# Kernel optimization log

Hardware: AMD Instinct MI355X
Metric: run time of the kernel (lower is better)

The kernel has to match this reference:

```python
import jax, jax.numpy as jnp
import numpy as np

B, T, C, H = 8, 2048, 1024, 64

def setup_inputs() -> dict:
    key = jax.random.key(0)
    kx, kq, kk, kv = jax.random.split(key, 4)
    scale = 1.0 / np.sqrt(C)
    return {
        "x": jax.random.normal(kx, (B, T, C), dtype=jnp.float32),
        "Wq": jax.random.normal(kq, (C, H), dtype=jnp.float32) * scale,
        "Wk": jax.random.normal(kk, (C, H), dtype=jnp.float32) * scale,
        "Wv": jax.random.normal(kv, (C, H), dtype=jnp.float32) * scale,
    }

def reference(x, Wq, Wk, Wv):
    # q,k,v: [B,T,H]
    q = jnp.einsum('btc,ch->bth', x, Wq)
    k = jnp.einsum('btc,ch->bth', x, Wk)
    v = jnp.einsum('btc,ch->bth', x, Wv)
    scale = k.shape[-1] ** -0.5
    wei = jnp.einsum('bth,bsh->bts', q, k) * scale  # [B,T,T]
    causal = jnp.tril(jnp.ones((x.shape[1], x.shape[1]), dtype=bool))
    wei = jnp.where(causal, wei, -jnp.inf)
    wei = jax.nn.softmax(wei, axis=-1)
    out = jnp.einsum('bts,bsh->bth', wei, v)  # [B,T,H]
    return out
```

## Files before the change

### kernel.cpp

```cpp
#include <hip/hip_runtime.h>

#define B_ 8
#define T_ 2048
#define C_ 1024
#define H_ 64

typedef __bf16 bf16x8 __attribute__((ext_vector_type(8)));
typedef float  f32x4  __attribute__((ext_vector_type(4)));
typedef unsigned short u16x8 __attribute__((ext_vector_type(8)));

__device__ __forceinline__ unsigned short f2bf(float f) {
    unsigned u = __builtin_bit_cast(unsigned, f);
    u += 0x8000u;
    return (unsigned short)(u >> 16);
}

__device__ __forceinline__ float bf2f(unsigned short v) {
    unsigned u = ((unsigned)v) << 16;
    return __builtin_bit_cast(float, u);
}

__device__ __forceinline__ unsigned pack2(float lo, float hi) {
    unsigned a = __builtin_bit_cast(unsigned, lo) + 0x8000u;
    unsigned b = __builtin_bit_cast(unsigned, hi) + 0x8000u;
    return (a >> 16) | (b & 0xffff0000u);
}

union U8 { unsigned u32[4]; u16x8 v; };

__device__ __forceinline__ u16x8 cvt8(float4 f0, float4 f1) {
    U8 r;
    r.u32[0] = pack2(f0.x, f0.y);
    r.u32[1] = pack2(f0.z, f0.w);
    r.u32[2] = pack2(f1.x, f1.y);
    r.u32[3] = pack2(f1.z, f1.w);
    return r.v;
}

__device__ __forceinline__ bf16x8 load8_bf(const unsigned short* p) {
    return __builtin_bit_cast(bf16x8, *(const u16x8*)p);
}


__global__ void cast_weights(const float* __restrict__ Wq,
                             const float* __restrict__ Wk,
                             const float* __restrict__ Wv,
                             unsigned short* __restrict__ Wtf) {
    int idx = blockIdx.x * blockDim.x + threadIdx.x;
    int n   = idx % 192;
    int c   = idx / 192;
    int w   = n >> 6;
    int h   = n & 63;
    const float* W = (w == 0) ? Wq : (w == 1) ? Wk : Wv;
    int nt = n >> 4, l16 = n & 15;
    int kc = c >> 5, quad = (c >> 3) & 3, j = c & 7;
    Wtf[(size_t)(nt * 32 + kc) * 512 + l16 * 32 + quad * 8 + j] =
        f2bf(W[(size_t)c * H_ + h]);
}

__global__ __launch_bounds__(512) void qkv_proj(
        const float* __restrict__ x,
        const unsigned short* __restrict__ Wtf,
        unsigned short* __restrict__ Qf,
        unsigned short* __restrict__ Kf,
        unsigned short* __restrict__ Vf) {
    __shared__ __attribute__((aligned(16))) unsigned short As_[32 * 1024];

    const int tid  = threadIdx.x;
    const int wave = tid >> 6;
    const int lane = tid & 63;
    const int l16  = lane & 15;
    const int quad = lane >> 4;
    const int ms   = wave >> 2;
    const int ns   = wave & 3;
    const size_t r0 = (size_t)blockIdx.x * 32;

#pragma unroll
    for (int i = 0; i < 8; i++) {
        int c   = i * 512 + tid;
        int row = c >> 7;
        int g   = c & 127;
        const float* p = x + (r0 + row) * C_ + g * 8;
        float4 f0 = *(const float4*)p;
        float4 f1 = *(const float4*)(p + 4);
        int off = row * 1024 + ((g & ~7) + ((g & 7) ^ (row & 7))) * 8;
        *(u16x8*)(&As_[off]) = cvt8(f0, f1);
    }
    __syncthreads();

    f32x4 acc[3];
#pragma unroll
    for (int i = 0; i < 3; i++) acc[i] = (f32x4){0.f, 0.f, 0.f, 0.f};

    const int arow = ms * 16 + l16;
    const int sw   = l16 & 7;
    const int loff = l16 * 32 + quad * 8;
    const unsigned short* wb = Wtf + (size_t)(ns * 3) * 32 * 512;

#pragma unroll 4
    for (int kc = 0; kc < 32; kc++) {
        int g = kc * 4 + quad;
        bf16x8 a = load8_bf(&As_[arow * 1024 + ((g & ~7) + ((g & 7) ^ sw)) * 8]);
#pragma unroll
        for (int i = 0; i < 3; i++) {
            bf16x8 b = load8_bf(wb + (size_t)(i * 32 + kc) * 512 + loff);
            acc[i] = __builtin_amdgcn_mfma_f32_16x16x32_bf16(a, b, acc[i], 0, 0, 0);
        }
    }

#pragma unroll
    for (int i = 0; i < 3; i++) {
        int nt = ns * 3 + i;
#pragma unroll
        for (int r = 0; r < 4; r++) {
            int row  = (int)r0 + ms * 16 + quad * 4 + r;
            int bb   = row >> 11;
            int tloc = row & (T_ - 1);
            unsigned short bv = f2bf(acc[i][r]);
            if (nt < 4) {
                int part  = nt >> 1;
                int quadf = (nt & 1) * 2 + (l16 >> 3);
                Qf[((size_t)(bb * 128 + (tloc >> 4)) * 2 + part) * 512
                   + (tloc & 15) * 32 + quadf * 8 + (l16 & 7)] = bv;
            } else if (nt < 8) {
                int nk    = nt - 4;
                int part  = nk >> 1;
                int quadf = (nk & 1) * 2 + (l16 >> 3);
                Kf[((size_t)(bb * 128 + (tloc >> 4)) * 2 + part) * 512
                   + (tloc & 15) * 32 + quadf * 8 + (l16 & 7)] = bv;
            } else {
                int ht  = nt - 8;
                int s32 = tloc >> 5;
                int w32 = tloc & 31;
                Vf[((size_t)(bb * 64 + s32) * 4 + ht) * 512
                   + l16 * 32 + (w32 >> 3) * 8 + (w32 & 7)] = bv;
            }
        }
    }
}

#define PROW 33
#define OMS2 66

__global__ __launch_bounds__(512) void attn(
        const unsigned short* __restrict__ Qf,
        const unsigned short* __restrict__ Kf,
        const unsigned short* __restrict__ Vf,
        float* __restrict__ out) {
    __shared__ unsigned int ps_[8 * 16 * PROW];
    __shared__ unsigned short Om_[8 * 16 * OMS2];
    __shared__ float mred_[8 * 16];
    __shared__ float lred_[8 * 16];

    const int tid  = threadIdx.x;
    const int wave = tid >> 6;
    const int lane = tid & 63;
    const int l16  = lane & 15;
    const int quad = lane >> 4;
    const int b    = blockIdx.x & 7;
    const int qt   = blockIdx.x >> 3;
    const int q0   = qt * 16;
    const int tdiag = qt >> 2;

    const int loff = l16 * 32 + quad * 8;

    const unsigned short* Qfb = Qf + (size_t)(b * 128 + qt) * 1024;
    bf16x8 qf0 = load8_bf(Qfb + loff);
    bf16x8 qf1 = load8_bf(Qfb + 512 + loff);

    f32x4 o[4];
#pragma unroll
    for (int i = 0; i < 4; i++) o[i] = (f32x4){0.f, 0.f, 0.f, 0.f};
    float m_run = -1e30f, l_run = 0.f;

    const float scale = 0.125f;
    const unsigned short* Kfb = Kf + (size_t)b * 128 * 1024;
    const unsigned short* Vfb = Vf + (size_t)b * 64 * 2048;
    unsigned int* Pw = &ps_[wave * 16 * PROW];

    for (int t = wave; t <= tdiag; t += 8) {
        bf16x8 vf[8];
#pragma unroll
        for (int ks = 0; ks < 2; ks++)
#pragma unroll
            for (int ht = 0; ht < 4; ht++)
                vf[ht * 2 + ks] = load8_bf(
                    Vfb + ((size_t)(t * 2 + ks) * 4 + ht) * 512 + loff);

        f32x4 s[4];
#pragma unroll
        for (int nt = 0; nt < 4; nt++) {
            const unsigned short* kp = Kfb + (size_t)(t * 4 + nt) * 1024;
            bf16x8 kf0 = load8_bf(kp + loff);
            bf16x8 kf1 = load8_bf(kp + 512 + loff);
            f32x4 z = (f32x4){0.f, 0.f, 0.f, 0.f};
            z = __builtin_amdgcn_mfma_f32_16x16x32_bf16(kf0, qf0, z, 0, 0, 0);
            z = __builtin_amdgcn_mfma_f32_16x16x32_bf16(kf1, qf1, z, 0, 0, 0);
            s[nt] = z;
        }

#pragma unroll
        for (int nt = 0; nt < 4; nt++)
#pragma unroll
            for (int r = 0; r < 4; r++) s[nt][r] *= scale;

        if (t == tdiag) {
#pragma unroll
            for (int nt = 0; nt < 4; nt++) {
#pragma unroll
                for (int r = 0; r < 4; r++) {
                    int key = t * 64 + nt * 16 + quad * 4 + r;
                    if (key > q0 + l16) s[nt][r] = -1e30f;
                }
            }
        }

        float mx;
        {
            float m0 = fmaxf(fmaxf(s[0][0], s[0][1]), fmaxf(s[0][2], s[0][3]));
            float m1 = fmaxf(fmaxf(s[1][0], s[1][1]), fmaxf(s[1][2], s[1][3]));
            float m2 = fmaxf(fmaxf(s[2][0], s[2][1]), fmaxf(s[2][2], s[2][3]));
            float m3 = fmaxf(fmaxf(s[3][0], s[3][1]), fmaxf(s[3][2], s[3][3]));
            mx = fmaxf(fmaxf(m0, m1), fmaxf(m2, m3));
        }
        mx = fmaxf(mx, __shfl_xor(mx, 16));
        mx = fmaxf(mx, __shfl_xor(mx, 32));
        const float m_new = fmaxf(m_run, mx);
        const float alpha = __expf(m_run - m_new);
        m_run = m_new;

        float rs = 0.f;
#pragma unroll
        for (int nt = 0; nt < 4; nt++) {
#pragma unroll
            for (int i = 0; i < 2; i++) {
                float p0 = __expf(s[nt][2 * i]     - m_new);
                float p1 = __expf(s[nt][2 * i + 1] - m_new);
                rs += p0 + p1;
                Pw[l16 * PROW + nt * 8 + quad * 2 + i] = pack2(p0, p1);
            }
        }
        rs += __shfl_xor(rs, 16);
        rs += __shfl_xor(rs, 32);
        l_run = l_run * alpha + rs;

#pragma unroll
        for (int ht = 0; ht < 4; ht++)
#pragma unroll
            for (int r = 0; r < 4; r++) o[ht][r] *= alpha;

#pragma unroll
        for (int ks = 0; ks < 2; ks++) {
            bf16x8 pB = __builtin_bit_cast(bf16x8,
                *(const u16x8*)(&Pw[l16 * PROW + ks * 16 + quad * 4]));
#pragma unroll
            for (int ht = 0; ht < 4; ht++)
                o[ht] = __builtin_amdgcn_mfma_f32_16x16x32_bf16(
                    vf[ht * 2 + ks], pB, o[ht], 0, 0, 0);
        }
    }

#pragma unroll
    for (int ht = 0; ht < 4; ht++)
#pragma unroll
        for (int r = 0; r < 4; r++)
            Om_[(wave * 16 + l16) * OMS2 + ht * 16 + quad * 4 + r] = f2bf(o[ht][r]);
    if (quad == 0) {
        mred_[wave * 16 + l16] = m_run;
        lred_[wave * 16 + l16] = l_run;
    }
    __syncthreads();

    const int hcol = tid & 63;
    const int qrow0 = tid >> 6;
#pragma unroll
    for (int qq = 0; qq < 2; qq++) {
        const int q = qrow0 + qq * 8;
        float M = -1e30f;
#pragma unroll
        for (int w = 0; w < 8; w++) M = fmaxf(M, mred_[w * 16 + q]);
        float lt = 0.f, ov = 0.f;
#pragma unroll
        for (int w = 0; w < 8; w++) {
            float e = __expf(mred_[w * 16 + q] - M);
            lt += e * lred_[w * 16 + q];
            ov += e * bf2f(Om_[(w * 16 + q) * OMS2 + hcol]);
        }
        out[((size_t)b * T_ + q0 + q) * H_ + hcol] = ov / lt;
    }
}

extern "C" void kernel_launch(void* const* d_in, const int* in_sizes, int n_in,
                              void* d_out, int out_size, void* d_ws, size_t ws_size,
                              hipStream_t stream) {
    const float* x  = (const float*)d_in[0];
    const float* Wq = (const float*)d_in[1];
    const float* Wk = (const float*)d_in[2];
    const float* Wv = (const float*)d_in[3];
    float* out = (float*)d_out;

    unsigned short* Qf  = (unsigned short*)d_ws;
    unsigned short* Kf  = Qf + (size_t)B_ * T_ * H_;
    unsigned short* Vf  = Kf + (size_t)B_ * T_ * H_;
    unsigned short* Wtf = Vf + (size_t)B_ * T_ * H_;

    cast_weights<<<(192 * C_) / 256, 256, 0, stream>>>(Wq, Wk, Wv, Wtf);
    qkv_proj<<<B_ * T_ / 32, 512, 0, stream>>>(x, Wtf, Qf, Kf, Vf);
    attn<<<B_ * (T_ / 16), 512, 0, stream>>>(Qf, Kf, Vf, out);
}
```

Measured before the change: 141.9 us.

## Reuse weight and K/V fragments across two row tiles and stage projection output

The QKV projection now uses 4 waves, each computing both 16-row halves. Each weight fragment therefore feeds two MFMAs, and x is staged in two K-halves to halve LDS use. Results are staged through LDS and written out as coalesced 16-byte stores instead of scattered 2-byte stores. Attention blocks now cover 32 queries with 4 waves, so each K/V fragment load serves two query groups. The cost is more registers per thread and fewer waves splitting the key range, which lengthens the per-wave serial loop.

Measured after the change: 141.4 us. No clear change (-0.3%).

```diff
diff --git a/kernel.cpp b/kernel.cpp
--- a/kernel.cpp
+++ b/kernel.cpp
@@ -53,104 +53,128 @@
     int h   = n & 63;
     const float* W = (w == 0) ? Wq : (w == 1) ? Wk : Wv;
     int nt = n >> 4, l16 = n & 15;
-    int kc = c >> 5, quad = (c >> 3) & 3, j = c & 7;
-    Wtf[(size_t)(nt * 32 + kc) * 512 + l16 * 32 + quad * 8 + j] =
+    int kk = c >> 5, quad = (c >> 3) & 3, j = c & 7;
+    Wtf[(size_t)(nt * 32 + kk) * 512 + l16 * 32 + quad * 8 + j] =
         f2bf(W[(size_t)c * H_ + h]);
 }
 
-__global__ __launch_bounds__(512) void qkv_proj(
+__global__ __launch_bounds__(256) void qkv_proj(
         const float* __restrict__ x,
         const unsigned short* __restrict__ Wtf,
         unsigned short* __restrict__ Qf,
         unsigned short* __restrict__ Kf,
         unsigned short* __restrict__ Vf) {
-    __shared__ __attribute__((aligned(16))) unsigned short As_[32 * 1024];
+    __shared__ __attribute__((aligned(16))) unsigned short As_[32 * 512];
 
     const int tid  = threadIdx.x;
-    const int wave = tid >> 6;
+    const int ns   = tid >> 6;
     const int lane = tid & 63;
     const int l16  = lane & 15;
     const int quad = lane >> 4;
-    const int ms   = wave >> 2;
-    const int ns   = wave & 3;
     const size_t r0 = (size_t)blockIdx.x * 32;
-
-#pragma unroll
-    for (int i = 0; i < 8; i++) {
-        int c   = i * 512 + tid;
-        int row = c >> 7;
-        int g   = c & 127;
-        const float* p = x + (r0 + row) * C_ + g * 8;
-        float4 f0 = *(const float4*)p;
-        float4 f1 = *(const float4*)(p + 4);
-        int off = row * 1024 + ((g & ~7) + ((g & 7) ^ (row & 7))) * 8;
-        *(u16x8*)(&As_[off]) = cvt8(f0, f1);
-    }
-    __syncthreads();
-
-    f32x4 acc[3];
-#pragma unroll
-    for (int i = 0; i < 3; i++) acc[i] = (f32x4){0.f, 0.f, 0.f, 0.f};
-
-    const int arow = ms * 16 + l16;
+    const int bb    = (int)(r0 >> 11);
+    const int tloc0 = (int)(r0 & (T_ - 1));
+    const int t16_0 = tloc0 >> 4;
+    const int s32   = tloc0 >> 5;
+
+    f32x4 acc[6];
+#pragma unroll
+    for (int i = 0; i < 6; i++) acc[i] = (f32x4){0.f, 0.f, 0.f, 0.f};
+
     const int sw   = l16 & 7;
     const int loff = l16 * 32 + quad * 8;
-    const unsigned short* wb = Wtf + (size_t)(ns * 3) * 32 * 512;
+
+    for (int p = 0; p < 2; p++) {
+        if (p) __syncthreads();
+#pragma unroll
+        for (int i = 0; i < 8; i++) {
+            int c   = i * 256 + tid;
+            int row = c >> 6;
+            int g   = c & 63;
+            const float* sp = x + (r0 + row) * C_ + p * 512 + g * 8;
+            float4 f0 = *(const float4*)sp;
+            float4 f1 = *(const float4*)(sp + 4);
+            int off = row * 512 + ((g & ~7) + ((g & 7) ^ (row & 7))) * 8;
+            *(u16x8*)(&As_[off]) = cvt8(f0, f1);
+        }
+        __syncthreads();
 
 #pragma unroll 4
-    for (int kc = 0; kc < 32; kc++) {
-        int g = kc * 4 + quad;
-        bf16x8 a = load8_bf(&As_[arow * 1024 + ((g & ~7) + ((g & 7) ^ sw)) * 8]);
-#pragma unroll
-        for (int i = 0; i < 3; i++) {
-            bf16x8 b = load8_bf(wb + (size_t)(i * 32 + kc) * 512 + loff);
-            acc[i] = __builtin_amdgcn_mfma_f32_16x16x32_bf16(a, b, acc[i], 0, 0, 0);
-        }
-    }
-
+        for (int kc = 0; kc < 16; kc++) {
+            int g  = kc * 4 + quad;
+            int gs = ((g & ~7) + ((g & 7) ^ sw)) * 8;
+            bf16x8 a0 = load8_bf(&As_[l16 * 512 + gs]);
+            bf16x8 a1 = load8_bf(&As_[(16 + l16) * 512 + gs]);
+            int kk = p * 16 + kc;
+#pragma unroll
+            for (int i = 0; i < 3; i++) {
+                bf16x8 b = load8_bf(Wtf + (size_t)((ns * 3 + i) * 32 + kk) * 512 + loff);
+                acc[i]     = __builtin_amdgcn_mfma_f32_16x16x32_bf16(a0, b, acc[i],     0, 0, 0);
+                acc[3 + i] = __builtin_amdgcn_mfma_f32_16x16x32_bf16(a1, b, acc[3 + i], 0, 0, 0);
+            }
+        }
+    }
+
+    __syncthreads();
+    unsigned short* E = As_;
 #pragma unroll
     for (int i = 0; i < 3; i++) {
         int nt = ns * 3 + i;
 #pragma unroll
-        for (int r = 0; r < 4; r++) {
-            int row  = (int)r0 + ms * 16 + quad * 4 + r;
-            int bb   = row >> 11;
-            int tloc = row & (T_ - 1);
-            unsigned short bv = f2bf(acc[i][r]);
-            if (nt < 4) {
-                int part  = nt >> 1;
-                int quadf = (nt & 1) * 2 + (l16 >> 3);
-                Qf[((size_t)(bb * 128 + (tloc >> 4)) * 2 + part) * 512
-                   + (tloc & 15) * 32 + quadf * 8 + (l16 & 7)] = bv;
-            } else if (nt < 8) {
-                int nk    = nt - 4;
-                int part  = nk >> 1;
-                int quadf = (nk & 1) * 2 + (l16 >> 3);
-                Kf[((size_t)(bb * 128 + (tloc >> 4)) * 2 + part) * 512
-                   + (tloc & 15) * 32 + quadf * 8 + (l16 & 7)] = bv;
-            } else {
-                int ht  = nt - 8;
-                int s32 = tloc >> 5;
-                int w32 = tloc & 31;
-                Vf[((size_t)(bb * 64 + s32) * 4 + ht) * 512
-                   + l16 * 32 + (w32 >> 3) * 8 + (w32 & 7)] = bv;
-            }
-        }
+        for (int msI = 0; msI < 2; msI++) {
+#pragma unroll
+            for (int r = 0; r < 4; r++) {
+                unsigned short bv = f2bf(acc[msI * 3 + i][r]);
+                int off;
+                int ch;
+                if (nt < 4) {
+                    ch  = msI * 2 + (nt >> 1);
+                    off = (quad * 4 + r) * 32 + ((nt & 1) * 2 + (l16 >> 3)) * 8 + (l16 & 7);
+                } else if (nt < 8) {
+                    int nk = nt - 4;
+                    ch  = 4 + msI * 2 + (nk >> 1);
+                    off = (quad * 4 + r) * 32 + ((nk & 1) * 2 + (l16 >> 3)) * 8 + (l16 & 7);
+                } else {
+                    int w32 = msI * 16 + quad * 4 + r;
+                    ch  = 8 + (nt - 8);
+                    off = l16 * 32 + (w32 >> 3) * 8 + (w32 & 7);
+                }
+                E[ch * 512 + off] = bv;
+            }
+        }
+    }
+    __syncthreads();
+
+#pragma unroll
+    for (int i = 0; i < 3; i++) {
+        int gi = i * 256 + tid;
+        int ch = gi >> 6;
+        int g  = gi & 63;
+        unsigned short* dst;
+        if (ch < 4) {
+            dst = Qf + ((size_t)(bb * 128 + t16_0 + (ch >> 1)) * 2 + (ch & 1)) * 512;
+        } else if (ch < 8) {
+            int c2 = ch - 4;
+            dst = Kf + ((size_t)(bb * 128 + t16_0 + (c2 >> 1)) * 2 + (c2 & 1)) * 512;
+        } else {
+            dst = Vf + ((size_t)(bb * 64 + s32) * 4 + (ch - 8)) * 512;
+        }
+        *(u16x8*)(dst + g * 8) = *(const u16x8*)(&E[ch * 512 + g * 8]);
     }
 }
 
 #define PROW 33
 #define OMS2 66
 
-__global__ __launch_bounds__(512) void attn(
+__global__ __launch_bounds__(256) void attn(
         const unsigned short* __restrict__ Qf,
         const unsigned short* __restrict__ Kf,
         const unsigned short* __restrict__ Vf,
         float* __restrict__ out) {
-    __shared__ unsigned int ps_[8 * 16 * PROW];
-    __shared__ unsigned short Om_[8 * 16 * OMS2];
-    __shared__ float mred_[8 * 16];
-    __shared__ float lred_[8 * 16];
+    __shared__ unsigned int ps_[4 * 32 * PROW];
+    __shared__ unsigned short Om_[4 * 32 * OMS2];
+    __shared__ float mred_[4][32];
+    __shared__ float lred_[4][32];
 
     const int tid  = threadIdx.x;
     const int wave = tid >> 6;
@@ -158,27 +182,31 @@
     const int l16  = lane & 15;
     const int quad = lane >> 4;
     const int b    = blockIdx.x & 7;
-    const int qt   = blockIdx.x >> 3;
-    const int q0   = qt * 16;
-    const int tdiag = qt >> 2;
+    const int qt32 = blockIdx.x >> 3;
+    const int q0   = qt32 * 32;
+    const int tdiag = qt32 >> 1;
 
     const int loff = l16 * 32 + quad * 8;
 
-    const unsigned short* Qfb = Qf + (size_t)(b * 128 + qt) * 1024;
-    bf16x8 qf0 = load8_bf(Qfb + loff);
-    bf16x8 qf1 = load8_bf(Qfb + 512 + loff);
-
-    f32x4 o[4];
-#pragma unroll
-    for (int i = 0; i < 4; i++) o[i] = (f32x4){0.f, 0.f, 0.f, 0.f};
-    float m_run = -1e30f, l_run = 0.f;
+    bf16x8 qf[2][2];
+#pragma unroll
+    for (int qg = 0; qg < 2; qg++) {
+        const unsigned short* Qfb = Qf + (size_t)((b * 128 + qt32 * 2 + qg) * 2) * 512;
+        qf[qg][0] = load8_bf(Qfb + loff);
+        qf[qg][1] = load8_bf(Qfb + 512 + loff);
+    }
+
+    f32x4 o[8];
+#pragma unroll
+    for (int i = 0; i < 8; i++) o[i] = (f32x4){0.f, 0.f, 0.f, 0.f};
+    float m_run[2] = {-1e30f, -1e30f}, l_run[2] = {0.f, 0.f};
 
     const float scale = 0.125f;
     const unsigned short* Kfb = Kf + (size_t)b * 128 * 1024;
     const unsigned short* Vfb = Vf + (size_t)b * 64 * 2048;
-    unsigned int* Pw = &ps_[wave * 16 * PROW];
-
-    for (int t = wave; t <= tdiag; t += 8) {
+    unsigned int* Pw = &ps_[wave * 32 * PROW];
+
+    for (int t = wave; t <= tdiag; t += 4) {
         bf16x8 vf[8];
 #pragma unroll
         for (int ks = 0; ks < 2; ks++)
@@ -187,104 +215,119 @@
                 vf[ht * 2 + ks] = load8_bf(
                     Vfb + ((size_t)(t * 2 + ks) * 4 + ht) * 512 + loff);
 
-        f32x4 s[4];
+        f32x4 s[2][4];
 #pragma unroll
         for (int nt = 0; nt < 4; nt++) {
             const unsigned short* kp = Kfb + (size_t)(t * 4 + nt) * 1024;
             bf16x8 kf0 = load8_bf(kp + loff);
             bf16x8 kf1 = load8_bf(kp + 512 + loff);
-            f32x4 z = (f32x4){0.f, 0.f, 0.f, 0.f};
-            z = __builtin_amdgcn_mfma_f32_16x16x32_bf16(kf0, qf0, z, 0, 0, 0);
-            z = __builtin_amdgcn_mfma_f32_16x16x32_bf16(kf1, qf1, z, 0, 0, 0);
-            s[nt] = z;
-        }
-
-#pragma unroll
-        for (int nt = 0; nt < 4; nt++)
-#pragma unroll
-            for (int r = 0; r < 4; r++) s[nt][r] *= scale;
+#pragma unroll
+            for (int qg = 0; qg < 2; qg++) {
+                f32x4 z = (f32x4){0.f, 0.f, 0.f, 0.f};
+                z = __builtin_amdgcn_mfma_f32_16x16x32_bf16(kf0, qf[qg][0], z, 0, 0, 0);
+                z = __builtin_amdgcn_mfma_f32_16x16x32_bf16(kf1, qf[qg][1], z, 0, 0, 0);
+                s[qg][nt] = z;
+            }
+        }
+
+#pragma unroll
+        for (int qg = 0; qg < 2; qg++)
+#pragma unroll
+            for (int nt = 0; nt < 4; nt++)
+#pragma unroll
+                for (int r = 0; r < 4; r++) s[qg][nt][r] *= scale;
 
         if (t == tdiag) {
 #pragma unroll
+            for (int qg = 0; qg < 2; qg++) {
+                int q = q0 + qg * 16 + l16;
+#pragma unroll
+                for (int nt = 0; nt < 4; nt++)
+#pragma unroll
+                    for (int r = 0; r < 4; r++) {
+                        int key = t * 64 + nt * 16 + quad * 4 + r;
+                        if (key > q) s[qg][nt][r] = -1e30f;
+                    }
+            }
+        }
+
+#pragma unroll
+        for (int qg = 0; qg < 2; qg++) {
+            float m0 = fmaxf(fmaxf(s[qg][0][0], s[qg][0][1]), fmaxf(s[qg][0][2], s[qg][0][3]));
+            float m1 = fmaxf(fmaxf(s[qg][1][0], s[qg][1][1]), fmaxf(s[qg][1][2], s[qg][1][3]));
+            float m2 = fmaxf(fmaxf(s[qg][2][0], s[qg][2][1]), fmaxf(s[qg][2][2], s[qg][2][3]));
+            float m3 = fmaxf(fmaxf(s[qg][3][0], s[qg][3][1]), fmaxf(s[qg][3][2], s[qg][3][3]));
+            float mx = fmaxf(fmaxf(m0, m1), fmaxf(m2, m3));
+            mx = fmaxf(mx, __shfl_xor(mx, 16));
+            mx = fmaxf(mx, __shfl_xor(mx, 32));
+            const float m_new = fmaxf(m_run[qg], mx);
+            const float alpha = __expf(m_run[qg] - m_new);
+            m_run[qg] = m_new;
+
+            float rs = 0.f;
+#pragma unroll
             for (int nt = 0; nt < 4; nt++) {
 #pragma unroll
-                for (int r = 0; r < 4; r++) {
-                    int key = t * 64 + nt * 16 + quad * 4 + r;
-                    if (key > q0 + l16) s[nt][r] = -1e30f;
+                for (int i = 0; i < 2; i++) {
+                    float p0 = __expf(s[qg][nt][2 * i]     - m_new);
+                    float p1 = __expf(s[qg][nt][2 * i + 1] - m_new);
+                    rs += p0 + p1;
+                    Pw[(qg * 16 + l16) * PROW + nt * 8 + quad * 2 + i] = pack2(p0, p1);
                 }
             }
-        }
-
-        float mx;
-        {
-            float m0 = fmaxf(fmaxf(s[0][0], s[0][1]), fmaxf(s[0][2], s[0][3]));
-            float m1 = fmaxf(fmaxf(s[1][0], s[1][1]), fmaxf(s[1][2], s[1][3]));
-            float m2 = fmaxf(fmaxf(s[2][0], s[2][1]), fmaxf(s[2][2], s[2][3]));
-            float m3 = fmaxf(fmaxf(s[3][0], s[3][1]), fmaxf(s[3][2], s[3][3]));
-            mx = fmaxf(fmaxf(m0, m1), fmaxf(m2, m3));
-        }
-        mx = fmaxf(mx, __shfl_xor(mx, 16));
-        mx = fmaxf(mx, __shfl_xor(mx, 32));
-        const float m_new = fmaxf(m_run, mx);
-        const float alpha = __expf(m_run - m_new);
-        m_run = m_new;
-
-        float rs = 0.f;
-#pragma unroll
-        for (int nt = 0; nt < 4; nt++) {
-#pragma unroll
-            for (int i = 0; i < 2; i++) {
-                float p0 = __expf(s[nt][2 * i]     - m_new);
-                float p1 = __expf(s[nt][2 * i + 1] - m_new);
-                rs += p0 + p1;
-                Pw[l16 * PROW + nt * 8 + quad * 2 + i] = pack2(p0, p1);
-            }
-        }
-        rs += __shfl_xor(rs, 16);
-        rs += __shfl_xor(rs, 32);
-        l_run = l_run * alpha + rs;
-
+            rs += __shfl_xor(rs, 16);
+            rs += __shfl_xor(rs, 32);
+            l_run[qg] = l_run[qg] * alpha + rs;
+
+#pragma unroll
+            for (int ht = 0; ht < 4; ht++)
+#pragma unroll
+                for (int r = 0; r < 4; r++) o[qg * 4 + ht][r] *= alpha;
+        }
+
+#pragma unroll
+        for (int ks = 0; ks < 2; ks++) {
+#pragma unroll
+            for (int qg = 0; qg < 2; qg++) {
+                bf16x8 pB = __builtin_bit_cast(bf16x8,
+                    *(const u16x8*)(&Pw[(qg * 16 + l16) * PROW + ks * 16 + quad * 4]));
+#pragma unroll
+                for (int ht = 0; ht < 4; ht++)
+                    o[qg * 4 + ht] = __builtin_amdgcn_mfma_f32_16x16x32_bf16(
+                        vf[ht * 2 + ks], pB, o[qg * 4 + ht], 0, 0, 0);
+            }
+        }
+    }
+
+#pragma unroll
+    for (int qg = 0; qg < 2; qg++) {
 #pragma unroll
         for (int ht = 0; ht < 4; ht++)
 #pragma unroll
-            for (int r = 0; r < 4; r++) o[ht][r] *= alpha;
-
-#pragma unroll
-        for (int ks = 0; ks < 2; ks++) {
-            bf16x8 pB = __builtin_bit_cast(bf16x8,
-                *(const u16x8*)(&Pw[l16 * PROW + ks * 16 + quad * 4]));
-#pragma unroll
-            for (int ht = 0; ht < 4; ht++)
-                o[ht] = __builtin_amdgcn_mfma_f32_16x16x32_bf16(
-                    vf[ht * 2 + ks], pB, o[ht], 0, 0, 0);
-        }
-    }
-
-#pragma unroll
-    for (int ht = 0; ht < 4; ht++)
-#pragma unroll
-        for (int r = 0; r < 4; r++)
-            Om_[(wave * 16 + l16) * OMS2 + ht * 16 + quad * 4 + r] = f2bf(o[ht][r]);
-    if (quad == 0) {
-        mred_[wave * 16 + l16] = m_run;
-        lred_[wave * 16 + l16] = l_run;
+            for (int r = 0; r < 4; r++)
+                Om_[(wave * 32 + qg * 16 + l16) * OMS2 + ht * 16 + quad * 4 + r] =
+                    f2bf(o[qg * 4 + ht][r]);
+        if (quad == 0) {
+            mred_[wave][qg * 16 + l16] = m_run[qg];
+            lred_[wave][qg * 16 + l16] = l_run[qg];
+        }
     }
     __syncthreads();
 
     const int hcol = tid & 63;
-    const int qrow0 = tid >> 6;
-#pragma unroll
-    for (int qq = 0; qq < 2; qq++) {
-        const int q = qrow0 + qq * 8;
+    const int qr0  = tid >> 6;
+#pragma unroll
+    for (int qq = 0; qq < 8; qq++) {
+        const int q = qr0 + qq * 4;
         float M = -1e30f;
 #pragma unroll
-        for (int w = 0; w < 8; w++) M = fmaxf(M, mred_[w * 16 + q]);
+        for (int w = 0; w < 4; w++) M = fmaxf(M, mred_[w][q]);
         float lt = 0.f, ov = 0.f;
 #pragma unroll
-        for (int w = 0; w < 8; w++) {
-            float e = __expf(mred_[w * 16 + q] - M);
-            lt += e * lred_[w * 16 + q];
-            ov += e * bf2f(Om_[(w * 16 + q) * OMS2 + hcol]);
+        for (int w = 0; w < 4; w++) {
+            float e = __expf(mred_[w][q] - M);
+            lt += e * lred_[w][q];
+            ov += e * bf2f(Om_[(w * 32 + q) * OMS2 + hcol]);
         }
         out[((size_t)b * T_ + q0 + q) * H_ + hcol] = ov / lt;
     }
@@ -305,6 +348,6 @@
     unsigned short* Wtf = Vf + (size_t)B_ * T_ * H_;
 
     cast_weights<<<(192 * C_) / 256, 256, 0, stream>>>(Wq, Wk, Wv, Wtf);
-    qkv_proj<<<B_ * T_ / 32, 512, 0, stream>>>(x, Wtf, Qf, Kf, Vf);
-    attn<<<B_ * (T_ / 16), 512, 0, stream>>>(Qf, Kf, Vf, out);
-}
+    qkv_proj<<<B_ * T_ / 32, 256, 0, stream>>>(x, Wtf, Qf, Kf, Vf);
+    attn<<<B_ * (T_ / 32), 256, 0, stream>>>(Qf, Kf, Vf, out);
+}
```
